# Performance work log

Hardware: AMD Instinct MI355X
Metric: run time of the kernel (lower is better)

Reference implementation:

```python
import jax, jax.numpy as jnp
import numpy as np

N_NODES = 100000
N_EDGES = 1600000
D = 128
L = 3
BN_EPS = 1e-5


def setup_inputs() -> dict:
    key = jax.random.key(0)
    ks = jax.random.split(key, 6)
    x = jax.random.normal(ks[0], (N_NODES, D), dtype=jnp.float32)
    edge_index = jax.random.randint(ks[1], (2, N_EDGES), 0, N_NODES, dtype=jnp.int64)
    Wl = jax.random.normal(ks[2], (L, D, D), dtype=jnp.float32) / np.sqrt(D)
    bl = jax.random.normal(ks[3], (L, D), dtype=jnp.float32) * 0.01
    Wr = jax.random.normal(ks[4], (L, D, D), dtype=jnp.float32) / np.sqrt(D)
    gamma = jnp.ones((L, D), dtype=jnp.float32)
    beta = jnp.zeros((L, D), dtype=jnp.float32)
    return {"x": x, "edge_index": edge_index, "Wl": Wl, "bl": bl,
            "Wr": Wr, "gamma": gamma, "beta": beta}


def _sage_layer(x, src, dst, inv_deg, Wl_i, bl_i, Wr_i, gamma_i, beta_i):
    # mean aggregation over incoming edges: scatter-add messages then divide by degree
    agg_sum = jax.ops.segment_sum(x[src], dst, num_segments=N_NODES)  # [N, D]
    agg = agg_sum * inv_deg[:, None]
    # SAGEConv: lin_l(agg) (with bias) + lin_r(x) (no bias)
    h = jnp.einsum('nd,hd->nh', agg, Wl_i) + bl_i + jnp.einsum('nd,hd->nh', x, Wr_i)
    # BatchNorm1d (training-mode batch stats, biased variance)
    mean = jnp.mean(h, axis=0)
    var = jnp.mean(jnp.square(h - mean), axis=0)
    h = (h - mean) * jax.lax.rsqrt(var + BN_EPS) * gamma_i + beta_i
    return jax.nn.relu(h)  # dropout is identity in eval mode


def reference(x, edge_index, Wl, bl, Wr, gamma, beta):
    src, dst = edge_index[0], edge_index[1]
    deg = jax.ops.segment_sum(jnp.ones((N_EDGES,), jnp.float32), dst,
                              num_segments=N_NODES)
    inv_deg = 1.0 / jnp.maximum(deg, 1.0)
    for i in range(L):
        h = _sage_layer(x, src, dst, inv_deg, Wl[i], bl[i], Wr[i], gamma[i], beta[i])
        if 0 < i < L - 1:  # middle layers get a scaled residual (shapes match)
            x = x + 0.5 * h
        else:
            x = h
    return x
```

## Files before the change

kernel.cpp:

```cpp
#include <hip/hip_runtime.h>

#define N_NODES 100000
#define N_EDGES 1600000
#define D 128
#define BN_EPS 1e-5f
#define N_GB ((N_NODES + 63) / 64)
#define NPART 8
#define FILL_BLOCKS 2048
#define NODES_PER_PART (N_NODES / NPART)
#define CAP 48

typedef short bf16x8 __attribute__((ext_vector_type(8)));
typedef float f32x4 __attribute__((ext_vector_type(4)));

__device__ inline unsigned short f32_to_bf16_rne(float f) {
    unsigned u = __builtin_bit_cast(unsigned, f);
    u += 0x7fffu + ((u >> 16) & 1u);
    return (unsigned short)(u >> 16);
}
__device__ inline float bf16lo_to_f32(unsigned v) { return __builtin_bit_cast(float, v << 16); }
__device__ inline float bf16hi_to_f32(unsigned v) { return __builtin_bit_cast(float, v & 0xffff0000u); }

__device__ inline void gload_lds16(const void* g, void* l) {
    __builtin_amdgcn_global_load_lds((const __attribute__((address_space(1))) unsigned*)g,
                                     (__attribute__((address_space(3))) unsigned*)l, 16, 0, 0);
}


__global__ __launch_bounds__(256) void k_prep(const float* __restrict__ x_in,
                                              const float* __restrict__ Wl, const float* __restrict__ Wr,
                                              unsigned short* __restrict__ xhi,
                                              unsigned short* __restrict__ wl_hi, unsigned short* __restrict__ wl_lo,
                                              unsigned short* __restrict__ wr_hi, unsigned short* __restrict__ wr_lo,
                                              int* __restrict__ cursor) {
    for (int idx = blockIdx.x * 256 + threadIdx.x; idx < N_NODES * 32; idx += FILL_BLOCKS * 256) {
        float4 v = ((const float4*)x_in)[idx];
        uint2 p;
        p.x = (unsigned)f32_to_bf16_rne(v.x) | ((unsigned)f32_to_bf16_rne(v.y) << 16);
        p.y = (unsigned)f32_to_bf16_rne(v.z) | ((unsigned)f32_to_bf16_rne(v.w) << 16);
        ((uint2*)xhi)[idx] = p;
    }
    for (int i = blockIdx.x * 256 + threadIdx.x; i < 2 * 3 * D * D; i += FILL_BLOCKS * 256) {
        const float* srcp = (i < 3 * D * D) ? Wl : Wr;
        int j = (i < 3 * D * D) ? i : i - 3 * D * D;
        float w = srcp[j];
        unsigned short h = f32_to_bf16_rne(w);
        float rem = w - bf16lo_to_f32((unsigned)h);
        if (i < 3 * D * D) { wl_hi[j] = h; wl_lo[j] = f32_to_bf16_rne(rem); }
        else               { wr_hi[j] = h; wr_lo[j] = f32_to_bf16_rne(rem); }
    }
    for (int i = blockIdx.x * 256 + threadIdx.x; i < N_NODES; i += FILL_BLOCKS * 256)
        cursor[i] = 0;
}

__global__ __launch_bounds__(256) void k_fill(const int* __restrict__ src, const int* __restrict__ dst,
                                              int* __restrict__ cursor, int* __restrict__ colidx) {
    const int part = blockIdx.x & (NPART - 1);
    const int lo = part * NODES_PER_PART;
    const int hi = lo + NODES_PER_PART;
    const int stride = (FILL_BLOCKS / NPART) * 256;
    for (int e = (blockIdx.x >> 3) * 256 + threadIdx.x; e < N_EDGES; e += stride) {
        int d = dst[e];
        if (d >= lo && d < hi) {
            int pos = atomicAdd(&cursor[d], 1);
            if (pos < CAP) colidx[d * CAP + pos] = src[e];
        }
    }
}


__global__ __launch_bounds__(256) void k_agg(const unsigned short* __restrict__ xhi,
                                             const int* __restrict__ cursor, const int* __restrict__ colidx,
                                             unsigned short* __restrict__ agghi) {
    const int wid = threadIdx.x >> 6;
    const int l = threadIdx.x & 63;
    const int n = blockIdx.x * 4 + wid;
    if (n >= N_NODES) return;
    const int degree = cursor[n];
    const int b = n * CAP;
    const int e = b + (degree < CAP ? degree : CAP);
    const int c8 = l & 15;
    const int g = l >> 4;
    const size_t coff = (size_t)c8 * 16;

    float acc[8];
#pragma unroll
    for (int k = 0; k < 8; k++) acc[k] = 0.f;

    int i = b;
    while (i < e) {
        int chunk = e - i; if (chunk > 64) chunk = 64;
        int myE = colidx[i + (l < chunk ? l : chunk - 1)];
        int j = 0;
        for (; j + 8 <= chunk; j += 8) {
            int s0 = __shfl(myE, j + g);
            int s1 = __shfl(myE, j + 4 + g);
            uint4 v0 = *(const uint4*)((const char*)xhi + (size_t)s0 * 256 + coff);
            uint4 v1 = *(const uint4*)((const char*)xhi + (size_t)s1 * 256 + coff);
            acc[0] += bf16lo_to_f32(v0.x); acc[1] += bf16hi_to_f32(v0.x);
            acc[2] += bf16lo_to_f32(v0.y); acc[3] += bf16hi_to_f32(v0.y);
            acc[4] += bf16lo_to_f32(v0.z); acc[5] += bf16hi_to_f32(v0.z);
            acc[6] += bf16lo_to_f32(v0.w); acc[7] += bf16hi_to_f32(v0.w);
            acc[0] += bf16lo_to_f32(v1.x); acc[1] += bf16hi_to_f32(v1.x);
            acc[2] += bf16lo_to_f32(v1.y); acc[3] += bf16hi_to_f32(v1.y);
            acc[4] += bf16lo_to_f32(v1.z); acc[5] += bf16hi_to_f32(v1.z);
            acc[6] += bf16lo_to_f32(v1.w); acc[7] += bf16hi_to_f32(v1.w);
        }
        for (; j + 4 <= chunk; j += 4) {
            int s0 = __shfl(myE, j + g);
            uint4 v0 = *(const uint4*)((const char*)xhi + (size_t)s0 * 256 + coff);
            acc[0] += bf16lo_to_f32(v0.x); acc[1] += bf16hi_to_f32(v0.x);
            acc[2] += bf16lo_to_f32(v0.y); acc[3] += bf16hi_to_f32(v0.y);
            acc[4] += bf16lo_to_f32(v0.z); acc[5] += bf16hi_to_f32(v0.z);
            acc[6] += bf16lo_to_f32(v0.w); acc[7] += bf16hi_to_f32(v0.w);
        }
        if (j < chunk) {
            int idx = j + g;
            int s0 = __shfl(myE, idx < chunk ? idx : chunk - 1);
            if (idx < chunk) {
                uint4 v0 = *(const uint4*)((const char*)xhi + (size_t)s0 * 256 + coff);
                acc[0] += bf16lo_to_f32(v0.x); acc[1] += bf16hi_to_f32(v0.x);
                acc[2] += bf16lo_to_f32(v0.y); acc[3] += bf16hi_to_f32(v0.y);
                acc[4] += bf16lo_to_f32(v0.z); acc[5] += bf16hi_to_f32(v0.z);
                acc[6] += bf16lo_to_f32(v0.w); acc[7] += bf16hi_to_f32(v0.w);
            }
        }
        i += chunk;
    }
#pragma unroll
    for (int k = 0; k < 8; k++) {
        acc[k] += __shfl_xor(acc[k], 16);
        acc[k] += __shfl_xor(acc[k], 32);
    }
    if (g == 0) {
        float idg = 1.0f / fmaxf((float)degree, 1.0f);
        uint4 p;
        p.x = (unsigned)f32_to_bf16_rne(acc[0] * idg) | ((unsigned)f32_to_bf16_rne(acc[1] * idg) << 16);
        p.y = (unsigned)f32_to_bf16_rne(acc[2] * idg) | ((unsigned)f32_to_bf16_rne(acc[3] * idg) << 16);
        p.z = (unsigned)f32_to_bf16_rne(acc[4] * idg) | ((unsigned)f32_to_bf16_rne(acc[5] * idg) << 16);
        p.w = (unsigned)f32_to_bf16_rne(acc[6] * idg) | ((unsigned)f32_to_bf16_rne(acc[7] * idg) << 16);
        *(uint4*)((char*)agghi + (size_t)n * 256 + coff) = p;
    }
}

__global__ __launch_bounds__(256, 2) void k_gemm(
    const unsigned short* __restrict__ agg_hi, const unsigned short* __restrict__ x_hi,
    const unsigned short* __restrict__ wl_hi, const unsigned short* __restrict__ wl_lo,
    const unsigned short* __restrict__ wr_hi, const unsigned short* __restrict__ wr_lo,
    const float* __restrict__ bl, unsigned short* __restrict__ h, float* __restrict__ partial) {
    __shared__ char lds[32768];
    const int t = threadIdx.x;
    const int w = t >> 6;
    const int l = t & 63;
    const int lr = l & 15;
    const int lg = l >> 4;
    const int base = blockIdx.x * 64;
    const int j0 = w * 32;

    {
#pragma unroll
        for (int i = 0; i < 8; i++) {
            int c = w * 8 + i;
            int ci = c & 15;
            int m = ci >> 2, kk = ci & 3;
            int n = base + m * 16 + lr;
            if (n > N_NODES - 1) n = N_NODES - 1;
            size_t goff = (size_t)n * 256 + kk * 64 + lg * 16;
            const char* srcp = ((c & 16) ? (const char*)x_hi : (const char*)agg_hi) + goff;
            gload_lds16(srcp, lds + c * 1024);
        }
    }

    f32x4 acc[4][2];
#pragma unroll
    for (int m = 0; m < 4; m++)
#pragma unroll
        for (int f = 0; f < 2; f++) acc[m][f] = (f32x4){0.f, 0.f, 0.f, 0.f};

#pragma unroll
    for (int seg = 0; seg < 2; seg++) {
        const unsigned short* WH = seg ? wr_hi : wl_hi;
        const unsigned short* WLo = seg ? wr_lo : wl_lo;
        bf16x8 wh[4][2], wlo[4][2];
#pragma unroll
        for (int kk = 0; kk < 4; kk++)
#pragma unroll
            for (int f = 0; f < 2; f++) {
                size_t wo = (size_t)(j0 + f * 16 + lr) * D + kk * 32 + lg * 8;
                wh[kk][f] = *(const bf16x8*)(WH + wo);
                wlo[kk][f] = *(const bf16x8*)(WLo + wo);
            }
        asm volatile("" :: "v"(wh[0][0]), "v"(wh[0][1]), "v"(wh[1][0]), "v"(wh[1][1]),
                           "v"(wh[2][0]), "v"(wh[2][1]), "v"(wh[3][0]), "v"(wh[3][1]));
        asm volatile("" :: "v"(wlo[0][0]), "v"(wlo[0][1]), "v"(wlo[1][0]), "v"(wlo[1][1]),
                           "v"(wlo[2][0]), "v"(wlo[2][1]), "v"(wlo[3][0]), "v"(wlo[3][1]));
        if (seg == 0) __syncthreads();
        const int tb = seg * 16384;
#pragma unroll
        for (int kk = 0; kk < 4; kk++) {
            bf16x8 a[4];
#pragma unroll
            for (int m = 0; m < 4; m++)
                a[m] = *(const bf16x8*)(lds + tb + (m * 4 + kk) * 1024 + l * 16);
#pragma unroll
            for (int f = 0; f < 2; f++)
#pragma unroll
                for (int m = 0; m < 4; m++) {
                    acc[m][f] = __builtin_amdgcn_mfma_f32_16x16x32_bf16(a[m], wh[kk][f], acc[m][f], 0, 0, 0);
                    acc[m][f] = __builtin_amdgcn_mfma_f32_16x16x32_bf16(a[m], wlo[kk][f], acc[m][f], 0, 0, 0);
                }
        }
    }

    float s1[2] = {0.f, 0.f}, s2[2] = {0.f, 0.f};
#pragma unroll
    for (int f = 0; f < 2; f++) {
        const int col = j0 + f * 16 + lr;
        const float bias = bl[col];
#pragma unroll
        for (int m = 0; m < 4; m++) {
#pragma unroll
            for (int r = 0; r < 4; r++) {
                int n = base + m * 16 + lg * 4 + r;
                if (n < N_NODES) {
                    float v = acc[m][f][r] + bias;
                    h[(size_t)n * D + col] = f32_to_bf16_rne(v);
                    s1[f] += v;
                    s2[f] += v * v;
                }
            }
        }
    }
#pragma unroll
    for (int f = 0; f < 2; f++) {
        s1[f] += __shfl_xor(s1[f], 16);
        s1[f] += __shfl_xor(s1[f], 32);
        s2[f] += __shfl_xor(s2[f], 16);
        s2[f] += __shfl_xor(s2[f], 32);
    }
    if (l < 16) {
        float* pp = partial + (size_t)blockIdx.x * 256;
        pp[j0 + l] = s1[0];
        pp[j0 + 16 + l] = s1[1];
        pp[128 + j0 + l] = s2[0];
        pp[128 + j0 + 16 + l] = s2[1];
    }
}

__global__ __launch_bounds__(256) void k_bnred(const float* __restrict__ partial, float* __restrict__ bn32) {
    int t = threadIdx.x;
    float s = 0.f;
    for (int b = blockIdx.x; b < N_GB; b += 32)
        s += partial[(size_t)b * 256 + t];
    bn32[blockIdx.x * 256 + t] = s;
}

__global__ __launch_bounds__(256) void k_apply(const unsigned short* __restrict__ h,
                                               const float* __restrict__ bn32,
                                               const float* __restrict__ gamma, const float* __restrict__ beta,
                                               const unsigned short* __restrict__ xres_hi,
                                               unsigned short* __restrict__ out_hi,
                                               float* __restrict__ out_f32, int mode) {
    __shared__ float sa[128], sc[128];
    int t = threadIdx.x;
    if (t < 128) {
        float m1 = 0.f, m2 = 0.f;
#pragma unroll 8
        for (int i = 0; i < 32; i++) {
            m1 += bn32[i * 256 + t];
            m2 += bn32[i * 256 + 128 + t];
        }
        float mean = m1 * (1.0f / N_NODES);
        float var = m2 * (1.0f / N_NODES) - mean * mean;
        float inv = rsqrtf(var + BN_EPS);
        float av = gamma[t] * inv;
        sa[t] = av;
        sc[t] = beta[t] - mean * av;
    }
    __syncthreads();
    int idx = blockIdx.x * 256 + t;
    if (idx >= N_NODES * 32) return;
    int c0 = (idx & 31) * 4;
    uint2 hv = ((const uint2*)h)[idx];
    float r0 = fmaxf(fmaf(bf16lo_to_f32(hv.x), sa[c0], sc[c0]), 0.f);
    float r1 = fmaxf(fmaf(bf16hi_to_f32(hv.x), sa[c0 + 1], sc[c0 + 1]), 0.f);
    float r2 = fmaxf(fmaf(bf16lo_to_f32(hv.y), sa[c0 + 2], sc[c0 + 2]), 0.f);
    float r3 = fmaxf(fmaf(bf16hi_to_f32(hv.y), sa[c0 + 3], sc[c0 + 3]), 0.f);
    if (mode == 1) {
        uint2 xv = ((const uint2*)xres_hi)[idx];
        r0 = fmaf(0.5f, r0, bf16lo_to_f32(xv.x));
        r1 = fmaf(0.5f, r1, bf16hi_to_f32(xv.x));
        r2 = fmaf(0.5f, r2, bf16lo_to_f32(xv.y));
        r3 = fmaf(0.5f, r3, bf16hi_to_f32(xv.y));
    }
    if (mode == 2) {
        ((float4*)out_f32)[idx] = make_float4(r0, r1, r2, r3);
    } else {
        uint2 p;
        p.x = (unsigned)f32_to_bf16_rne(r0) | ((unsigned)f32_to_bf16_rne(r1) << 16);
        p.y = (unsigned)f32_to_bf16_rne(r2) | ((unsigned)f32_to_bf16_rne(r3) << 16);
        ((uint2*)out_hi)[idx] = p;
    }
}


extern "C" void kernel_launch(void* const* d_in, const int* in_sizes, int n_in,
                              void* d_out, int out_size, void* d_ws, size_t ws_size,
                              hipStream_t stream) {
    const float* x_in = (const float*)d_in[0];
    const int* ei = (const int*)d_in[1];
    const float* Wl = (const float*)d_in[2];
    const float* bl = (const float*)d_in[3];
    const float* Wr = (const float*)d_in[4];
    const float* gamma = (const float*)d_in[5];
    const float* beta = (const float*)d_in[6];
    float* out = (float*)d_out;

    char* ws = (char*)d_ws;
    unsigned short* xhiA = (unsigned short*)ws; ws += (size_t)N_NODES * D * 2;
    unsigned short* xhiB = (unsigned short*)ws; ws += (size_t)N_NODES * D * 2;
    unsigned short* agghi = (unsigned short*)ws; ws += (size_t)N_NODES * D * 2;
    int* cursor = (int*)ws; ws += (size_t)N_NODES * 4;
    int* colidx = (int*)ws; ws += (size_t)N_NODES * CAP * 4;
    unsigned short* wl_hi = (unsigned short*)ws; ws += (size_t)3 * D * D * 2;
    unsigned short* wl_lo = (unsigned short*)ws; ws += (size_t)3 * D * D * 2;
    unsigned short* wr_hi = (unsigned short*)ws; ws += (size_t)3 * D * D * 2;
    unsigned short* wr_lo = (unsigned short*)ws; ws += (size_t)3 * D * D * 2;
    float* partial = (float*)ws; ws += (size_t)N_GB * 256 * 4;
    float* bn32 = (float*)ws; ws += 32 * 256 * 4;

    const int* src = ei;
    const int* dst = ei + N_EDGES;

    k_prep<<<FILL_BLOCKS, 256, 0, stream>>>(x_in, Wl, Wr, xhiA, wl_hi, wl_lo, wr_hi, wr_lo, cursor);
    k_fill<<<FILL_BLOCKS, 256, 0, stream>>>(src, dst, cursor, colidx);

    unsigned short* xin[3] = { xhiA, xhiB, xhiA };
    unsigned short* xout[3] = { xhiB, xhiA, (unsigned short*)0 };
    int mode[3] = { 0, 1, 2 };

    for (int i = 0; i < 3; i++) {
        k_agg<<<(N_NODES + 3) / 4, 256, 0, stream>>>(xin[i], cursor, colidx, agghi);
        k_gemm<<<N_GB, 256, 0, stream>>>(agghi, xin[i],
                                         wl_hi + (size_t)i * D * D, wl_lo + (size_t)i * D * D,
                                         wr_hi + (size_t)i * D * D, wr_lo + (size_t)i * D * D,
                                         bl + (size_t)i * D, agghi, partial);
        k_bnred<<<32, 256, 0, stream>>>(partial, bn32);
        k_apply<<<(N_NODES * 32 + 255) / 256, 256, 0, stream>>>(agghi, bn32,
                                                                gamma + (size_t)i * D, beta + (size_t)i * D,
                                                                xin[i], xout[i], out, mode[i]);
    }
}
```

Baseline: 499.9 us.

## Bucket edges by destination partition before building per-node adjacency lists

```diff
diff --git a/kernel.cpp b/kernel.cpp
--- a/kernel.cpp
+++ b/kernel.cpp
@@ -9,6 +9,7 @@
 #define FILL_BLOCKS 2048
 #define NODES_PER_PART (N_NODES / NPART)
 #define CAP 48
+#define PCAP 210000
 
 typedef short bf16x8 __attribute__((ext_vector_type(8)));
 typedef float f32x4 __attribute__((ext_vector_type(4)));
@@ -32,7 +33,7 @@
                                               unsigned short* __restrict__ xhi,
                                               unsigned short* __restrict__ wl_hi, unsigned short* __restrict__ wl_lo,
                                               unsigned short* __restrict__ wr_hi, unsigned short* __restrict__ wr_lo,
-                                              int* __restrict__ cursor) {
+                                              int* __restrict__ cursor, int* __restrict__ gcur) {
     for (int idx = blockIdx.x * 256 + threadIdx.x; idx < N_NODES * 32; idx += FILL_BLOCKS * 256) {
         float4 v = ((const float4*)x_in)[idx];
         uint2 p;
@@ -51,20 +52,57 @@
     }
     for (int i = blockIdx.x * 256 + threadIdx.x; i < N_NODES; i += FILL_BLOCKS * 256)
         cursor[i] = 0;
-}
-
-__global__ __launch_bounds__(256) void k_fill(const int* __restrict__ src, const int* __restrict__ dst,
-                                              int* __restrict__ cursor, int* __restrict__ colidx) {
-    const int part = blockIdx.x & (NPART - 1);
-    const int lo = part * NODES_PER_PART;
-    const int hi = lo + NODES_PER_PART;
+    if (blockIdx.x == 0 && threadIdx.x < NPART) gcur[threadIdx.x] = 0;
+}
+
+__global__ __launch_bounds__(256) void k_split(const int* __restrict__ src, const int* __restrict__ dst,
+                                               int* __restrict__ gcur, unsigned* __restrict__ pairbuf) {
+    __shared__ int cnt[NPART];
+    __shared__ int base[NPART];
+    const int t = threadIdx.x;
+    if (t < NPART) cnt[t] = 0;
+    __syncthreads();
+    unsigned pk[4];
+    int part[4], pos[4];
+    const int e0 = blockIdx.x * 256 + t;
+#pragma unroll
+    for (int r = 0; r < 4; r++) {
+        int e = e0 + r * (FILL_BLOCKS * 256);
+        part[r] = -1;
+        if (e < N_EDGES) {
+            int d = dst[e];
+            int s = src[e];
+            int p = d / NODES_PER_PART;
+            part[r] = p;
+            pos[r] = atomicAdd(&cnt[p], 1);
+            pk[r] = ((unsigned)(d - p * NODES_PER_PART) << 17) | (unsigned)s;
+        }
+    }
+    __syncthreads();
+    if (t < NPART) base[t] = atomicAdd(&gcur[t], cnt[t]);
+    __syncthreads();
+#pragma unroll
+    for (int r = 0; r < 4; r++) {
+        if (part[r] >= 0) {
+            unsigned idx = (unsigned)(base[part[r]] + pos[r]);
+            if (idx < PCAP) pairbuf[(size_t)part[r] * PCAP + idx] = pk[r];
+        }
+    }
+}
+
+__global__ __launch_bounds__(256) void k_fill2(const unsigned* __restrict__ pairbuf,
+                                               const int* __restrict__ gcur,
+                                               int* __restrict__ cursor, int* __restrict__ colidx) {
+    const int p = blockIdx.x & (NPART - 1);
+    const int m = gcur[p];
     const int stride = (FILL_BLOCKS / NPART) * 256;
-    for (int e = (blockIdx.x >> 3) * 256 + threadIdx.x; e < N_EDGES; e += stride) {
-        int d = dst[e];
-        if (d >= lo && d < hi) {
-            int pos = atomicAdd(&cursor[d], 1);
-            if (pos < CAP) colidx[d * CAP + pos] = src[e];
-        }
+    const unsigned* pb = pairbuf + (size_t)p * PCAP;
+    const int dbase = p * NODES_PER_PART;
+    for (int i = (blockIdx.x >> 3) * 256 + threadIdx.x; i < m; i += stride) {
+        unsigned pk = pb[i];
+        int d = dbase + (int)(pk >> 17);
+        int pos = atomicAdd(&cursor[d], 1);
+        if (pos < CAP) colidx[d * CAP + pos] = (int)(pk & 0x1FFFFu);
     }
 }
 
@@ -322,6 +360,8 @@
     unsigned short* agghi = (unsigned short*)ws; ws += (size_t)N_NODES * D * 2;
     int* cursor = (int*)ws; ws += (size_t)N_NODES * 4;
     int* colidx = (int*)ws; ws += (size_t)N_NODES * CAP * 4;
+    unsigned* pairbuf = (unsigned*)ws; ws += (size_t)NPART * PCAP * 4;
+    int* gcur = (int*)ws; ws += 64;
     unsigned short* wl_hi = (unsigned short*)ws; ws += (size_t)3 * D * D * 2;
     unsigned short* wl_lo = (unsigned short*)ws; ws += (size_t)3 * D * D * 2;
     unsigned short* wr_hi = (unsigned short*)ws; ws += (size_t)3 * D * D * 2;
@@ -332,8 +372,10 @@
     const int* src = ei;
     const int* dst = ei + N_EDGES;
 
-    k_prep<<<FILL_BLOCKS, 256, 0, stream>>>(x_in, Wl, Wr, xhiA, wl_hi, wl_lo, wr_hi, wr_lo, cursor);
-    k_fill<<<FILL_BLOCKS, 256, 0, stream>>>(src, dst, cursor, colidx);
+    k_prep<<<FILL_BLOCKS, 256, 0, stream>>>(x_in, Wl, Wr, xhiA, wl_hi, wl_lo, wr_hi, wr_lo,
+                                            cursor, gcur);
+    k_split<<<FILL_BLOCKS, 256, 0, stream>>>(src, dst, gcur, pairbuf);
+    k_fill2<<<FILL_BLOCKS, 256, 0, stream>>>(pairbuf, gcur, cursor, colidx);
 
     unsigned short* xin[3] = { xhiA, xhiB, xhiA };
     unsigned short* xout[3] = { xhiB, xhiA, (unsigned short*)0 };
```

Result: slower. 526.1 us (+5.2%).
